# Kernel optimization log

Hardware: AMD Instinct MI355X
Metric: run time of the kernel (lower is better)

Reference implementation:

```python
import jax, jax.numpy as jnp
import numpy as np

# Transformer config constants (from init_kwargs)
SRF = 3.0                 # spatial_receptive_field
SRF2 = SRF * SRF
ALPHA = 2.0
BETA = 8.0
GAMMA = 16.0
RES = jnp.array([0.5, 0.5, 0.5], dtype=jnp.float32)   # relative_positional_gresolution
N_BUCKETS = 2 * 8 + 1                                  # 2*beta + 1 = 17
MUL = jnp.array([N_BUCKETS ** 2, N_BUCKETS, 1], dtype=jnp.float32)  # [289,17,1]
SLICES_PER_ROT = 2


def setup_inputs() -> dict:
    key = jax.random.key(0)
    k1, k2 = jax.random.split(key)
    N = 3072
    # LiDAR-like point coordinates in a 10m cube; receptive field 3.0 makes radius filter selective
    xyz = jax.random.uniform(k1, (N, 3), dtype=jnp.float32) * 10.0
    # grid columns: [batch, block, gx, gy, gz]; values < 128 per the torch assert
    grid = jax.random.randint(k2, (N, 5), 0, 8, dtype=jnp.int32)
    return {"xyz": xyz, "grid": grid}


def _bucket_base(x):
    # from_dxyz_to_bucket_base, res.size(0)==3 branch
    x = x / RES
    x_abs = jnp.abs(x)
    log_ratio = jnp.log(jnp.maximum(x_abs, 1e-6) / ALPHA) / np.log(GAMMA / ALPHA)
    sup = jnp.minimum(jnp.round(ALPHA - (BETA - ALPHA) * log_ratio), BETA)
    sup = jnp.sign(x) * sup
    return BETA + jnp.where(x_abs <= ALPHA, jnp.round(x), sup)


def reference(xyz, grid):
    # no-kvp path of jit_compute_interactions, expressed as dense [N,N] pair masks
    batch = grid[:, 0]
    block = grid[:, 1]
    coords = grid[:, 2:]            # grid_look[:, 1:]

    # batch equality filter (meshgrid + batch==batch)
    batch_eq = batch[:, None] == batch[None, :]
    # causal block filter: block[iq] <= block[ik]
    block_le = block[:, None] <= block[None, :]

    # force_keep_neighbours: adjacent voxels within the same block
    coord_adj = jnp.max(jnp.abs(coords[:, None, :] - coords[None, :, :]), axis=-1) <= 1
    forcekeep = coord_adj & (block[:, None] == block[None, :])

    # coarse spatial hash on xy: ceil(xy / srf), neighbor cells only
    xy_coarse = jnp.ceil(xyz[:, :2] / SRF).astype(jnp.int32)
    keep_coarse = jnp.max(jnp.abs(xy_coarse[:, None, :] - xy_coarse[None, :, :]), axis=-1) <= 1

    # pairwise deltas (torch uses fp16 here; fp32 kept for numerical clarity) [N,N,3]
    dxyz = xyz[:, None, :] - xyz[None, :, :]
    keepr = jnp.sum(dxyz * dxyz, axis=-1) <= SRF2

    mask = batch_eq & block_le & (forcekeep | keep_coarse) & (forcekeep | keepr)

    dxyz_m = jnp.where(mask[..., None], dxyz, 0.0)

    # from_dxyz_to_bucket_mul: log-bucketize each axis, flatten via mul_buckets
    buckets = jnp.sum(MUL * _bucket_base(dxyz_m), axis=-1).astype(jnp.int32)
    buckets = jnp.where(mask, buckets, 0)

    # dscanid = scanid[ik] - scanid[iq], scanid = block // slices_per_rotation
    scanid = block // SLICES_PER_ROT
    dscanid = jnp.where(mask, scanid[None, :] - scanid[:, None], 0)

    return dxyz_m, buckets, dscanid, mask
```

## Files before the change

kernel.cpp:

```cpp
#include <hip/hip_runtime.h>
#include <cmath>


__device__ __forceinline__ float bucket_base(float v) {
    const float x  = v * 2.0f;
    const float xa = fabsf(x);
    const float rnd = rintf(x);
    const float inv_den = (float)2.0794415416798357;
    const float lr  = logf(fmaxf(xa, 1e-6f) * 0.5f) / inv_den;
    float sup = fminf(rintf(2.0f - 6.0f * lr), 8.0f);
    const float s = (x > 0.0f) ? 1.0f : ((x < 0.0f) ? -1.0f : 0.0f);
    sup = s * sup;
    return 8.0f + ((xa <= 2.0f) ? rnd : sup);
}

__global__ __launch_bounds__(256) void pair_kernel(
    const float* __restrict__ xyz, const int* __restrict__ grid,
    float* __restrict__ out, int N) {
#pragma clang fp contract(off)
    const int j = blockIdx.x * blockDim.x + threadIdx.x;
    const int i = blockIdx.y;
    if (j >= N) return;

    const float xi = xyz[3 * i + 0];
    const float yi = xyz[3 * i + 1];
    const float zi = xyz[3 * i + 2];
    const int   bat_i = grid[5 * i + 0];
    const int   blk_i = grid[5 * i + 1];
    const int   c0i   = grid[5 * i + 2];
    const int   c1i   = grid[5 * i + 3];
    const int   c2i   = grid[5 * i + 4];

    const float xj = xyz[3 * j + 0];
    const float yj = xyz[3 * j + 1];
    const float zj = xyz[3 * j + 2];
    const int   bat_j = grid[5 * j + 0];
    const int   blk_j = grid[5 * j + 1];
    const int   c0j   = grid[5 * j + 2];
    const int   c1j   = grid[5 * j + 3];
    const int   c2j   = grid[5 * j + 4];

    const bool batch_eq = (bat_i == bat_j);
    const bool block_le = (blk_i <= blk_j);
    const int  cadj = max(max(abs(c0i - c0j), abs(c1i - c1j)), abs(c2i - c2j));
    const bool forcekeep = (cadj <= 1) && (blk_i == blk_j);

    const int xci = (int)ceilf(xi / 3.0f);
    const int yci = (int)ceilf(yi / 3.0f);
    const int xcj = (int)ceilf(xj / 3.0f);
    const int ycj = (int)ceilf(yj / 3.0f);
    const bool keep_coarse = max(abs(xci - xcj), abs(yci - ycj)) <= 1;

    const float dx = xi - xj;
    const float dy = yi - yj;
    const float dz = zi - zj;
    const float d2 = dx * dx + dy * dy + dz * dz;
    const bool keepr = (d2 <= 9.0f);

    const bool mask = batch_eq && block_le &&
                      (forcekeep || keep_coarse) && (forcekeep || keepr);

    const float dxm = mask ? dx : 0.0f;
    const float dym = mask ? dy : 0.0f;
    const float dzm = mask ? dz : 0.0f;

    const float b0 = bucket_base(dxm);
    const float b1 = bucket_base(dym);
    const float b2 = bucket_base(dzm);
    const float bsum = (289.0f * b0 + 17.0f * b1) + b2;
    const int bucket = mask ? (int)bsum : 0;

    const int dscan = mask ? ((blk_j >> 1) - (blk_i >> 1)) : 0;

    const size_t NN   = (size_t)N * (size_t)N;
    const size_t base = (size_t)i * (size_t)N + (size_t)j;

    const size_t o0 = base * 3;
    out[o0 + 0] = dxm;
    out[o0 + 1] = dym;
    out[o0 + 2] = dzm;
    out[NN * 3 + base] = (float)bucket;
    out[NN * 4 + base] = (float)dscan;
    out[NN * 5 + base] = mask ? 1.0f : 0.0f;
}

extern "C" void kernel_launch(void* const* d_in, const int* in_sizes, int n_in,
                              void* d_out, int out_size, void* d_ws, size_t ws_size,
                              hipStream_t stream) {
    const float* xyz  = (const float*)d_in[0];
    const int*   grid = (const int*)d_in[1];
    float*       out  = (float*)d_out;
    const int N = in_sizes[0] / 3;

    const int BLOCK = 256;
    dim3 gdim((N + BLOCK - 1) / BLOCK, N, 1);
    pair_kernel<<<gdim, dim3(BLOCK, 1, 1), 0, stream>>>(xyz, grid, out, N);
}
```

Baseline: 229.8 us.

## Process four j-points per thread with float4 loads/stores and skip masked bucket math

Each thread now handles four consecutive j points, loading coordinates and grid rows as vector float4/int4 loads and writing all outputs as float4 stores. Wavefronts where no pair passes the mask write zeros directly and return, and bucket computation is done only for masked lanes, with the log path taken only when the scaled delta exceeds 2. This targets store throughput and wasted transcendental work on a write-bound kernel. It assumes N is divisible by 4 and that the buffers are 16-byte aligned.

```diff
diff --git a/kernel.cpp b/kernel.cpp
--- a/kernel.cpp
+++ b/kernel.cpp
@@ -5,83 +5,112 @@
 __device__ __forceinline__ float bucket_base(float v) {
     const float x  = v * 2.0f;
     const float xa = fabsf(x);
-    const float rnd = rintf(x);
-    const float inv_den = (float)2.0794415416798357;
-    const float lr  = logf(fmaxf(xa, 1e-6f) * 0.5f) / inv_den;
-    float sup = fminf(rintf(2.0f - 6.0f * lr), 8.0f);
-    const float s = (x > 0.0f) ? 1.0f : ((x < 0.0f) ? -1.0f : 0.0f);
-    sup = s * sup;
-    return 8.0f + ((xa <= 2.0f) ? rnd : sup);
+    if (xa <= 2.0f) {
+        return 8.0f + rintf(x);
+    }
+    const float lr = logf(fmaxf(xa, 1e-6f) * 0.5f) / 2.0794415416798357f;
+    const float sup = fminf(rintf(2.0f - 6.0f * lr), 8.0f);
+    return 8.0f + ((x > 0.0f) ? sup : -sup);
 }
 
 __global__ __launch_bounds__(256) void pair_kernel(
     const float* __restrict__ xyz, const int* __restrict__ grid,
     float* __restrict__ out, int N) {
 #pragma clang fp contract(off)
-    const int j = blockIdx.x * blockDim.x + threadIdx.x;
-    const int i = blockIdx.y;
-    if (j >= N) return;
+    const int jq = blockIdx.x * blockDim.x + threadIdx.x;
+    const int j0 = jq << 2;
+    const int i  = blockIdx.y;
+    if (j0 >= N) return;
 
     const float xi = xyz[3 * i + 0];
     const float yi = xyz[3 * i + 1];
     const float zi = xyz[3 * i + 2];
-    const int   bat_i = grid[5 * i + 0];
-    const int   blk_i = grid[5 * i + 1];
-    const int   c0i   = grid[5 * i + 2];
-    const int   c1i   = grid[5 * i + 3];
-    const int   c2i   = grid[5 * i + 4];
-
-    const float xj = xyz[3 * j + 0];
-    const float yj = xyz[3 * j + 1];
-    const float zj = xyz[3 * j + 2];
-    const int   bat_j = grid[5 * j + 0];
-    const int   blk_j = grid[5 * j + 1];
-    const int   c0j   = grid[5 * j + 2];
-    const int   c1j   = grid[5 * j + 3];
-    const int   c2j   = grid[5 * j + 4];
-
-    const bool batch_eq = (bat_i == bat_j);
-    const bool block_le = (blk_i <= blk_j);
-    const int  cadj = max(max(abs(c0i - c0j), abs(c1i - c1j)), abs(c2i - c2j));
-    const bool forcekeep = (cadj <= 1) && (blk_i == blk_j);
-
+    const int bat_i = grid[5 * i + 0];
+    const int blk_i = grid[5 * i + 1];
+    const int c0i = grid[5 * i + 2];
+    const int c1i = grid[5 * i + 3];
+    const int c2i = grid[5 * i + 4];
     const int xci = (int)ceilf(xi / 3.0f);
     const int yci = (int)ceilf(yi / 3.0f);
-    const int xcj = (int)ceilf(xj / 3.0f);
-    const int ycj = (int)ceilf(yj / 3.0f);
-    const bool keep_coarse = max(abs(xci - xcj), abs(yci - ycj)) <= 1;
+    const int scan_i = blk_i >> 1;
 
-    const float dx = xi - xj;
-    const float dy = yi - yj;
-    const float dz = zi - zj;
-    const float d2 = dx * dx + dy * dy + dz * dz;
-    const bool keepr = (d2 <= 9.0f);
+    const float4* pv = reinterpret_cast<const float4*>(xyz + (size_t)3 * j0);
+    const float4 p0 = pv[0], p1 = pv[1], p2 = pv[2];
+    const int4* gv = reinterpret_cast<const int4*>(grid + (size_t)5 * j0);
+    const int4 g0 = gv[0], g1 = gv[1], g2 = gv[2], g3 = gv[3], g4 = gv[4];
 
-    const bool mask = batch_eq && block_le &&
-                      (forcekeep || keep_coarse) && (forcekeep || keepr);
+    const float jx[4]  = {p0.x, p0.w, p1.z, p2.y};
+    const float jy[4]  = {p0.y, p1.x, p1.w, p2.z};
+    const float jz[4]  = {p0.z, p1.y, p2.x, p2.w};
+    const int   jbat[4] = {g0.x, g1.y, g2.z, g3.w};
+    const int   jblk[4] = {g0.y, g1.z, g2.w, g4.x};
+    const int   jc0[4]  = {g0.z, g1.w, g3.x, g4.y};
+    const int   jc1[4]  = {g0.w, g2.x, g3.y, g4.z};
+    const int   jc2[4]  = {g1.x, g2.y, g3.z, g4.w};
 
-    const float dxm = mask ? dx : 0.0f;
-    const float dym = mask ? dy : 0.0f;
-    const float dzm = mask ? dz : 0.0f;
-
-    const float b0 = bucket_base(dxm);
-    const float b1 = bucket_base(dym);
-    const float b2 = bucket_base(dzm);
-    const float bsum = (289.0f * b0 + 17.0f * b1) + b2;
-    const int bucket = mask ? (int)bsum : 0;
-
-    const int dscan = mask ? ((blk_j >> 1) - (blk_i >> 1)) : 0;
+    float dxm[4], dym[4], dzm[4];
+    bool  mk[4];
+    bool  any = false;
+#pragma unroll
+    for (int k = 0; k < 4; ++k) {
+        const float dx = xi - jx[k];
+        const float dy = yi - jy[k];
+        const float dz = zi - jz[k];
+        const bool batch_eq = (bat_i == jbat[k]);
+        const bool block_le = (blk_i <= jblk[k]);
+        const int  cadj = max(max(abs(c0i - jc0[k]), abs(c1i - jc1[k])),
+                              abs(c2i - jc2[k]));
+        const bool forcekeep = (cadj <= 1) && (blk_i == jblk[k]);
+        const int xcj = (int)ceilf(jx[k] / 3.0f);
+        const int ycj = (int)ceilf(jy[k] / 3.0f);
+        const bool keep_coarse = max(abs(xci - xcj), abs(yci - ycj)) <= 1;
+        const float d2 = dx * dx + dy * dy + dz * dz;
+        const bool keepr = (d2 <= 9.0f);
+        const bool m = batch_eq && block_le &&
+                       (forcekeep || keep_coarse) && (forcekeep || keepr);
+        mk[k] = m;
+        any |= m;
+        dxm[k] = m ? dx : 0.0f;
+        dym[k] = m ? dy : 0.0f;
+        dzm[k] = m ? dz : 0.0f;
+    }
 
     const size_t NN   = (size_t)N * (size_t)N;
-    const size_t base = (size_t)i * (size_t)N + (size_t)j;
+    const size_t base = (size_t)i * (size_t)N + (size_t)j0;
+    float4* o_dxyz = reinterpret_cast<float4*>(out + 3 * base);
+    float4* o_bkt  = reinterpret_cast<float4*>(out + NN * 3 + base);
+    float4* o_dsc  = reinterpret_cast<float4*>(out + NN * 4 + base);
+    float4* o_msk  = reinterpret_cast<float4*>(out + NN * 5 + base);
 
-    const size_t o0 = base * 3;
-    out[o0 + 0] = dxm;
-    out[o0 + 1] = dym;
-    out[o0 + 2] = dzm;
-    out[NN * 3 + base] = (float)bucket;
-    out[NN * 4 + base] = (float)dscan;
-    out[NN * 5 + base] = mask ? 1.0f : 0.0f;
+    if (__ballot(any ? 1 : 0) == 0ULL) {
+        const float4 z = make_float4(0.0f, 0.0f, 0.0f, 0.0f);
+        o_dxyz[0] = z; o_dxyz[1] = z; o_dxyz[2] = z;
+        o_bkt[0]  = z; o_dsc[0]  = z; o_msk[0]  = z;
+        return;
+    }
+
+    float bf[4], df[4], mf[4];
+#pragma unroll
+    for (int k = 0; k < 4; ++k) {
+        if (mk[k]) {
+            const float b0 = bucket_base(dxm[k]);
+            const float b1 = bucket_base(dym[k]);
+            const float b2 = bucket_base(dzm[k]);
+            const float bsum = (289.0f * b0 + 17.0f * b1) + b2;
+            bf[k] = (float)(int)bsum;
+            df[k] = (float)((jblk[k] >> 1) - scan_i);
+            mf[k] = 1.0f;
+        } else {
+            bf[k] = 0.0f; df[k] = 0.0f; mf[k] = 0.0f;
+        }
+    }
+
+    o_dxyz[0] = make_float4(dxm[0], dym[0], dzm[0], dxm[1]);
+    o_dxyz[1] = make_float4(dym[1], dzm[1], dxm[2], dym[2]);
+    o_dxyz[2] = make_float4(dzm[2], dxm[3], dym[3], dzm[3]);
+    o_bkt[0]  = make_float4(bf[0], bf[1], bf[2], bf[3]);
+    o_dsc[0]  = make_float4(df[0], df[1], df[2], df[3]);
+    o_msk[0]  = make_float4(mf[0], mf[1], mf[2], mf[3]);
 }
 
 extern "C" void kernel_launch(void* const* d_in, const int* in_sizes, int n_in,
@@ -93,6 +122,7 @@
     const int N = in_sizes[0] / 3;
 
     const int BLOCK = 256;
-    dim3 gdim((N + BLOCK - 1) / BLOCK, N, 1);
+    const int jquads = N / 4;
+    dim3 gdim((jquads + BLOCK - 1) / BLOCK, N, 1);
     pair_kernel<<<gdim, dim3(BLOCK, 1, 1), 0, stream>>>(xyz, grid, out, N);
 }
```

Result: faster. 219.6 us (-4.4%).
